# Kernel tuning notes

Measured on AMD Instinct MI355X. Metric: run time of the kernel, lower is better.

## Reference

```python
import jax, jax.numpy as jnp
import numpy as np

D_MODEL, N_HEAD, N_KV_HEAD, D_HEAD = 1024, 16, 4, 64


def rotate_half(x):
    x1, x2 = x[..., : x.shape[-1] // 2], x[..., x.shape[-1] // 2:]
    return jnp.concatenate((-x2, x1), axis=-1)


def rope_cos_sin(seq_len, dim, dtype=jnp.float32):
    inv_freq = 1.0 / (10000.0 ** (jnp.arange(0, dim, 2, dtype=jnp.float32) / dim))
    t = jnp.arange(seq_len, dtype=jnp.float32)
    freqs = jnp.einsum('i,j->ij', t, inv_freq)          # [S, dim/2]
    emb = jnp.concatenate((freqs, freqs), axis=-1)       # [S, dim]
    return jnp.cos(emb).astype(dtype), jnp.sin(emb).astype(dtype)


def setup_inputs() -> dict:
    key = jax.random.key(0)
    ks = jax.random.split(key, 5)
    B, S = 2, 2048
    scale = 0.02
    return {
        'x': jax.random.normal(ks[0], (B, S, D_MODEL), dtype=jnp.float32),
        'Wq': jax.random.normal(ks[1], (D_MODEL, N_HEAD * D_HEAD), dtype=jnp.float32) * scale,
        'Wk': jax.random.normal(ks[2], (D_MODEL, N_KV_HEAD * D_HEAD), dtype=jnp.float32) * scale,
        'Wv': jax.random.normal(ks[3], (D_MODEL, N_KV_HEAD * D_HEAD), dtype=jnp.float32) * scale,
        'Wo': jax.random.normal(ks[4], (N_HEAD * D_HEAD, D_MODEL), dtype=jnp.float32) * scale,
    }


def reference(x, Wq, Wk, Wv, Wo):
    B, S, _ = x.shape
    scale = 1.0 / np.sqrt(D_HEAD)
    # projections -> [B, H, S, Dh]
    q = (x @ Wq).reshape(B, S, N_HEAD, D_HEAD).transpose(0, 2, 1, 3)
    k = (x @ Wk).reshape(B, S, N_KV_HEAD, D_HEAD).transpose(0, 2, 1, 3)
    v = (x @ Wv).reshape(B, S, N_KV_HEAD, D_HEAD).transpose(0, 2, 1, 3)
    cos, sin = rope_cos_sin(S, D_HEAD, x.dtype)          # [S, Dh]
    q = q * cos + rotate_half(q) * sin
    k = k * cos + rotate_half(k) * sin
    rep = N_HEAD // N_KV_HEAD
    k = jnp.repeat(k, rep, axis=1)                       # [B, H, S, Dh]
    v = jnp.repeat(v, rep, axis=1)
    scores = jnp.einsum('bhqd,bhkd->bhqk', q, k) * scale # [B, H, S, S]
    causal = jnp.triu(jnp.ones((S, S), dtype=bool), k=1)
    scores = jnp.where(causal, -jnp.inf, scores)
    probs = jax.nn.softmax(scores, axis=-1)
    ctx = jnp.einsum('bhqk,bhkd->bhqd', probs, v)        # [B, H, S, Dh]
    ctx = ctx.transpose(0, 2, 1, 3).reshape(B, S, N_HEAD * D_HEAD)
    return ctx @ Wo
```

## Files before the change

kernel.cpp:

```cpp
#include <hip/hip_runtime.h>
#include <hip/hip_bf16.h>
#include <cstdint>
#include <math.h>

#define S_LEN 2048
#define DM 1024
#define NQKV 1536
#define MROWS 4096

typedef __attribute__((ext_vector_type(8))) short short8;
typedef __attribute__((ext_vector_type(4))) short short4v;
typedef __attribute__((ext_vector_type(4))) float f32x4;

#define MEMBAR() __asm__ __volatile__("" ::: "memory")

#define QFOLD 0.18033688011112042f

__device__ __forceinline__ short f2bf(float x) {
  union { float f; uint32_t u; } v; v.f = x;
  uint32_t r = (v.u + 0x7fffu + ((v.u >> 16) & 1u)) >> 16;
  return (short)(uint16_t)r;
}

__device__ __forceinline__ uint32_t pk2(float a, float b) {
  __hip_bfloat162 h = __float22bfloat162_rn(make_float2(a, b));
  union { __hip_bfloat162 h2; uint32_t u; } cv; cv.h2 = h;
  return cv.u;
}

__global__ void f32_to_bf16_vec(const float* __restrict__ in, short* __restrict__ out, int n4) {
  int i = blockIdx.x * blockDim.x + threadIdx.x;
  if (i < n4) {
    float4 v = ((const float4*)in)[i];
    short4 o;
    o.x = f2bf(v.x); o.y = f2bf(v.y); o.z = f2bf(v.z); o.w = f2bf(v.w);
    ((short4*)out)[i] = o;
  }
}

__global__ __launch_bounds__(256) void transpose_f32_bf16(const float* __restrict__ src,
    short* __restrict__ dst, int R, int C) {
  __shared__ short T[64 * 72];
  const int r0 = blockIdx.x * 64, c0 = blockIdx.y * 64;
  const int tid = threadIdx.x;
  #pragma unroll
  for (int i = 0; i < 4; ++i) {
    int chunk = tid + i * 256;
    int r = chunk >> 4, cc = (chunk & 15) * 4;
    float4 v = *(const float4*)&src[(size_t)(r0 + r) * C + c0 + cc];
    T[(cc + 0) * 72 + r] = f2bf(v.x);
    T[(cc + 1) * 72 + r] = f2bf(v.y);
    T[(cc + 2) * 72 + r] = f2bf(v.z);
    T[(cc + 3) * 72 + r] = f2bf(v.w);
  }
  __syncthreads();
  #pragma unroll
  for (int i = 0; i < 2; ++i) {
    int chunk = tid + i * 256;
    int rr = chunk >> 3, kk = (chunk & 7) * 8;
    *(uint4*)&dst[(size_t)(c0 + rr) * R + r0 + kk] = *(uint4*)&T[rr * 72 + kk];
  }
}

#define BM 128
#define BN 128
#define BKT 64

__global__ __launch_bounds__(256) void gemm_bf16(const short* __restrict__ A,
    const short* __restrict__ BT, float* __restrict__ C, int M, int N, int K) {
  __shared__ short As[BM * BKT];
  __shared__ short Bs[BN * BKT];
  const int tid = threadIdx.x;
  const int wave = tid >> 6, lane = tid & 63;
  const int quad = lane >> 4, l15 = lane & 15;
  const int wm = (wave >> 1) * 64, wn = (wave & 1) * 64;
  const int m0 = blockIdx.y * BM, n0 = blockIdx.x * BN;

  const int sr = wave * 32 + (lane >> 3);
  const int scol = (lane & 7) * 8;

  f32x4 acc[4][4] = {};

  for (int k0 = 0; k0 < K; k0 += BKT) {
    __syncthreads();
    #pragma unroll
    for (int j = 0; j < 4; ++j) {
      const int r = sr + j * 8;
      __builtin_amdgcn_global_load_lds(
          (const __attribute__((address_space(1))) void*)&A[(size_t)(m0 + r) * K + k0 + scol],
          (__attribute__((address_space(3))) void*)&As[(wave * 4 + j) * 512],
          16, 0, 0);
      __builtin_amdgcn_global_load_lds(
          (const __attribute__((address_space(1))) void*)&BT[(size_t)(n0 + r) * K + k0 + scol],
          (__attribute__((address_space(3))) void*)&Bs[(wave * 4 + j) * 512],
          16, 0, 0);
    }
    __syncthreads();
    #pragma unroll
    for (int ks = 0; ks < 2; ++ks) {
      short8 af[4], bfr[4];
      #pragma unroll
      for (int mi = 0; mi < 4; ++mi)
        af[mi] = *(const short8*)&As[(wm + mi*16 + l15)*BKT + ks*32 + quad*8];
      #pragma unroll
      for (int ni = 0; ni < 4; ++ni)
        bfr[ni] = *(const short8*)&Bs[(wn + ni*16 + l15)*BKT + ks*32 + quad*8];
      #pragma unroll
      for (int mi = 0; mi < 4; ++mi)
        #pragma unroll
        for (int ni = 0; ni < 4; ++ni)
          acc[mi][ni] = __builtin_amdgcn_mfma_f32_16x16x32_bf16(af[mi], bfr[ni], acc[mi][ni], 0, 0, 0);
    }
  }
  #pragma unroll
  for (int mi = 0; mi < 4; ++mi)
    #pragma unroll
    for (int ni = 0; ni < 4; ++ni)
      #pragma unroll
      for (int r = 0; r < 4; ++r)
        C[(size_t)(m0 + wm + mi*16 + quad*4 + r)*N + (n0 + wn + ni*16 + l15)] = acc[mi][ni][r];
}

__global__ void rope_kernel(const float* __restrict__ qkv, short* __restrict__ Qb,
                            short* __restrict__ Kb, short* __restrict__ Vb) {
  __shared__ float csn[64];
  const int row = blockIdx.x;
  const int s = row & (S_LEN - 1);
  const int tid = threadIdx.x;
  const float* rp = qkv + (size_t)row * NQKV;
  if (tid < 32) {
    float inv = exp2f(-(float)tid * 0.41524101186092029f);
    float ang = (float)s * inv;
    csn[tid] = cosf(ang);
    csn[tid + 32] = sinf(ang);
  }
  __syncthreads();
  #pragma unroll
  for (int i = 0; i < 2; ++i) {
    int p = tid + i * 256;
    int hh = p >> 5, j = p & 31;
    float cs = csn[j], sn = csn[j + 32];
    float x1 = rp[hh*64 + j], x2 = rp[hh*64 + j + 32];
    Qb[(size_t)row*1024 + hh*64 + j]      = f2bf((x1*cs - x2*sn) * QFOLD);
    Qb[(size_t)row*1024 + hh*64 + j + 32] = f2bf((x2*cs + x1*sn) * QFOLD);
  }
  if (tid < 128) {
    int hh = tid >> 5, j = tid & 31;
    float cs = csn[j], sn = csn[j + 32];
    float x1 = rp[1024 + hh*64 + j], x2 = rp[1024 + hh*64 + j + 32];
    Kb[(size_t)row*256 + hh*64 + j]      = f2bf(x1*cs - x2*sn);
    Kb[(size_t)row*256 + hh*64 + j + 32] = f2bf(x2*cs + x1*sn);
  }
  Vb[(size_t)row*256 + tid] = f2bf(rp[1280 + tid]);
}

__global__ __launch_bounds__(256) void transpose_v(const short* __restrict__ Vb,
                                                   short* __restrict__ Vt) {
  __shared__ short T[64 * 72];
  const int s0 = blockIdx.x * 64;
  const int bh = blockIdx.y;
  const int b = bh >> 2, kvh = bh & 3;
  const int tid = threadIdx.x;
  #pragma unroll
  for (int i = 0; i < 2; ++i) {
    int chunk = tid + i * 256;
    int r = chunk >> 3, c = (chunk & 7) * 8;
    short8 v = *(const short8*)&Vb[(size_t)(b*S_LEN + s0 + r)*256 + kvh*64 + c];
    #pragma unroll
    for (int t = 0; t < 8; ++t) T[(c + t) * 72 + r] = v[t];
  }
  __syncthreads();
  #pragma unroll
  for (int i = 0; i < 2; ++i) {
    int chunk = tid + i * 256;
    int rr = chunk >> 3, kk = (chunk & 7) * 8;
    *(uint4*)&Vt[(size_t)(bh*64 + rr)*S_LEN + s0 + kk] = *(uint4*)&T[rr * 72 + kk];
  }
}

#define PSTR 136

__global__ __launch_bounds__(256, 2) void fattn6(const short* __restrict__ Qb,
    const short* __restrict__ Kb, const short* __restrict__ Vt, short* __restrict__ Ctx) {
  __shared__ short Ks[128 * 72];
  __shared__ short Vts[64 * PSTR];
  __shared__ short Ps[4 * 16 * PSTR];
  const int idx = blockIdx.x;
  const int pi  = idx & 15;
  const int h   = (idx >> 4) & 15;
  const int b   = idx >> 8;
  const int kvh = h >> 2;
  const int tid = threadIdx.x, wave = tid >> 6, lane = tid & 63;
  const int quad = lane >> 4, l15 = lane & 15;
  const int roff = wave * 16;
  const size_t qbase  = (size_t)b * S_LEN * 1024;
  const size_t kbase  = (size_t)b * S_LEN * 256;
  const size_t vtbase = (size_t)(b*4 + kvh) * 64 * S_LEN;
  short* Psw = Ps + wave * 16 * PSTR;

  for (int half = 0; half < 2; ++half) {
    const int jt = half ? (31 - pi) : pi;
    const int q0 = jt * 64;
    const int ntiles = (jt >> 1) + 1;
    const int qrow = q0 + roff + l15;

    const short* qp = &Qb[qbase + (size_t)(q0 + roff + l15)*1024 + h*64 + quad*8];
    short8 qf0 = *(const short8*)qp;
    short8 qf1 = *(const short8*)(qp + 32);

    f32x4 O[4] = {};
    float ll = 0.f;

    short8 kreg[4], vreg[4];
    #pragma unroll
    for (int i = 0; i < 4; ++i) {
      int chunk = tid + i * 256;
      int kr = chunk >> 3, kc = (chunk & 7) * 8;
      kreg[i] = *(const short8*)&Kb[kbase + (size_t)kr*256 + kvh*64 + kc];
      int vr = chunk >> 4, vc = (chunk & 15) * 8;
      vreg[i] = *(const short8*)&Vt[vtbase + (size_t)vr*S_LEN + vc];
    }

    for (int t = 0; t < ntiles; ++t) {
      const int k0 = t * 128;
      __syncthreads();
      #pragma unroll
      for (int i = 0; i < 4; ++i) {
        int chunk = tid + i * 256;
        int kr = chunk >> 3, kc = (chunk & 7) * 8;
        *(short8*)&Ks[kr*72 + kc] = kreg[i];
        int vr = chunk >> 4, vc = (chunk & 15) * 8;
        *(short8*)&Vts[vr*PSTR + vc] = vreg[i];
      }
      __syncthreads();
      if (t + 1 < ntiles) {
        const int kn = (t + 1) * 128;
        #pragma unroll
        for (int i = 0; i < 4; ++i) {
          int chunk = tid + i * 256;
          int kr = chunk >> 3, kc = (chunk & 7) * 8;
          kreg[i] = *(const short8*)&Kb[kbase + (size_t)(kn + kr)*256 + kvh*64 + kc];
          int vr = chunk >> 4, vc = (chunk & 15) * 8;
          vreg[i] = *(const short8*)&Vt[vtbase + (size_t)vr*S_LEN + kn + vc];
        }
      }

      f32x4 sc[8];
      #pragma unroll
      for (int nt = 0; nt < 8; ++nt) {
        short8 kf0 = *(const short8*)&Ks[(nt*16 + l15)*72 + quad*8];
        short8 kf1 = *(const short8*)&Ks[(nt*16 + l15)*72 + 32 + quad*8];
        f32x4 a = {0.f, 0.f, 0.f, 0.f};
        a = __builtin_amdgcn_mfma_f32_16x16x32_bf16(kf0, qf0, a, 0, 0, 0);
        a = __builtin_amdgcn_mfma_f32_16x16x32_bf16(kf1, qf1, a, 0, 0, 0);
        sc[nt] = a;
      }
      if (t == ntiles - 1) {
        #pragma unroll
        for (int nt = 0; nt < 8; ++nt)
          #pragma unroll
          for (int r = 0; r < 4; ++r)
            if (k0 + nt*16 + quad*4 + r > qrow) sc[nt][r] = -1e30f;
      }
      #pragma unroll
      for (int nt = 0; nt < 8; ++nt) {
        float p0 = exp2f(sc[nt][0]);
        float p1 = exp2f(sc[nt][1]);
        float p2 = exp2f(sc[nt][2]);
        float p3 = exp2f(sc[nt][3]);
        ll += (p0 + p1) + (p2 + p3);
        union { uint2 uu; short4v s; } pkc;
        pkc.uu.x = pk2(p0, p1); pkc.uu.y = pk2(p2, p3);
        *(short4v*)&Psw[l15*PSTR + nt*16 + quad*4] = pkc.s;
      }
      MEMBAR();
      #pragma unroll
      for (int ks = 0; ks < 4; ++ks) {
        short8 a = *(const short8*)&Psw[l15*PSTR + ks*32 + quad*8];
        #pragma unroll
        for (int d = 0; d < 4; ++d) {
          short8 bv = *(const short8*)&Vts[(d*16 + l15)*PSTR + ks*32 + quad*8];
          O[d] = __builtin_amdgcn_mfma_f32_16x16x32_bf16(a, bv, O[d], 0, 0, 0);
        }
      }
    }

    ll += __shfl_xor(ll, 16, 64);
    ll += __shfl_xor(ll, 32, 64);
    #pragma unroll
    for (int r = 0; r < 4; ++r) {
      float lr = __shfl(ll, quad*4 + r, 64);
      float inv = 1.0f / lr;
      #pragma unroll
      for (int d = 0; d < 4; ++d) {
        int qr = q0 + roff + quad*4 + r;
        Ctx[qbase + (size_t)qr*1024 + h*64 + d*16 + l15] = f2bf(O[d][r] * inv);
      }
    }
  }
}

extern "C" void kernel_launch(void* const* d_in, const int* in_sizes, int n_in,
                              void* d_out, int out_size, void* d_ws, size_t ws_size,
                              hipStream_t stream) {
  const float* x  = (const float*)d_in[0];
  const float* Wq = (const float*)d_in[1];
  const float* Wk = (const float*)d_in[2];
  const float* Wv = (const float*)d_in[3];
  const float* Wo = (const float*)d_in[4];
  float* out = (float*)d_out;

  char* w = (char*)d_ws;
  short* Xb    = (short*)w;  w += (size_t)MROWS * DM * 2;
  short* WcatT = (short*)w;  w += (size_t)NQKV * DM * 2;
  short* WoT   = (short*)w;  w += (size_t)DM * DM * 2;
  float* QKVf  = (float*)w;  w += (size_t)MROWS * NQKV * 4;
  short* Qbuf  = (short*)w;  w += (size_t)MROWS * DM * 2;
  short* Kbuf  = (short*)w;  w += (size_t)MROWS * 256 * 2;
  short* Vbuf  = (short*)w;  w += (size_t)MROWS * 256 * 2;
  short* Vt    = (short*)w;  w += (size_t)8 * 64 * S_LEN * 2;
  short* Ctx   = (short*)QKVf;

  f32_to_bf16_vec<<<dim3(4096), dim3(256), 0, stream>>>(x, Xb, MROWS * DM / 4);
  transpose_f32_bf16<<<dim3(16, 16), dim3(256), 0, stream>>>(Wq, WcatT, 1024, 1024);
  transpose_f32_bf16<<<dim3(16, 4),  dim3(256), 0, stream>>>(Wk, WcatT + (size_t)1024*1024, 1024, 256);
  transpose_f32_bf16<<<dim3(16, 4),  dim3(256), 0, stream>>>(Wv, WcatT + (size_t)1280*1024, 1024, 256);
  transpose_f32_bf16<<<dim3(16, 16), dim3(256), 0, stream>>>(Wo, WoT, 1024, 1024);

  gemm_bf16<<<dim3(NQKV / BN, MROWS / BM), dim3(256), 0, stream>>>(Xb, WcatT, QKVf, MROWS, NQKV, DM);
  rope_kernel<<<dim3(MROWS), dim3(256), 0, stream>>>(QKVf, Qbuf, Kbuf, Vbuf);
  transpose_v<<<dim3(32, 8), dim3(256), 0, stream>>>(Vbuf, Vt);
  fattn6<<<dim3(512), dim3(256), 0, stream>>>(Qbuf, Kbuf, Vt, Ctx);
  gemm_bf16<<<dim3(DM / BN, MROWS / BM), dim3(256), 0, stream>>>(Ctx, WoT, out, MROWS, DM, DM);
}
```

Before: 195.5 us.

## Fuse RoPE and bf16 conversion into QKV GEMM epilogue; merge weight transposes

The QKV projection GEMM now applies RoPE, the Q scale fold and bf16 conversion in its epilogue and writes Q, K and V directly. This removes the fp32 QKV intermediate buffer and the separate rope kernel pass over it. The four weight-transpose launches are also merged into one launch. In exchange, each output element recomputes sin/cos per row in the GEMM epilogue, and the Ctx buffer now gets its own workspace region.

```diff
diff --git a/kernel.cpp b/kernel.cpp
--- a/kernel.cpp
+++ b/kernel.cpp
@@ -15,6 +15,7 @@
 #define MEMBAR() __asm__ __volatile__("" ::: "memory")
 
 #define QFOLD 0.18033688011112042f
+#define L2I 0.41524101186092029f
 
 __device__ __forceinline__ short f2bf(float x) {
   union { float f; uint32_t u; } v; v.f = x;
@@ -38,10 +39,17 @@
   }
 }
 
-__global__ __launch_bounds__(256) void transpose_f32_bf16(const float* __restrict__ src,
-    short* __restrict__ dst, int R, int C) {
+__global__ __launch_bounds__(256) void transpose_all(const float* __restrict__ Wq,
+    const float* __restrict__ Wk, const float* __restrict__ Wv, const float* __restrict__ Wo,
+    short* __restrict__ WcatT, short* __restrict__ WoT) {
   __shared__ short T[64 * 72];
-  const int r0 = blockIdx.x * 64, c0 = blockIdx.y * 64;
+  int t = blockIdx.x;
+  const float* src; short* dst; int C;
+  if (t < 256)      { src = Wq; dst = WcatT;                        C = 1024; }
+  else if (t < 320) { t -= 256; src = Wk; dst = WcatT + 1024*1024;  C = 256; }
+  else if (t < 384) { t -= 320; src = Wv; dst = WcatT + 1280*1024;  C = 256; }
+  else              { t -= 384; src = Wo; dst = WoT;                C = 1024; }
+  const int r0 = (t & 15) * 64, c0 = (t >> 4) * 64;
   const int tid = threadIdx.x;
   #pragma unroll
   for (int i = 0; i < 4; ++i) {
@@ -58,7 +66,7 @@
   for (int i = 0; i < 2; ++i) {
     int chunk = tid + i * 256;
     int rr = chunk >> 3, kk = (chunk & 7) * 8;
-    *(uint4*)&dst[(size_t)(c0 + rr) * R + r0 + kk] = *(uint4*)&T[rr * 72 + kk];
+    *(uint4*)&dst[(size_t)(c0 + rr) * 1024 + r0 + kk] = *(uint4*)&T[rr * 72 + kk];
   }
 }
 
@@ -66,8 +74,9 @@
 #define BN 128
 #define BKT 64
 
-__global__ __launch_bounds__(256) void gemm_bf16(const short* __restrict__ A,
-    const short* __restrict__ BT, float* __restrict__ C, int M, int N, int K) {
+__global__ __launch_bounds__(256) void gemm_qkv_rope(const short* __restrict__ A,
+    const short* __restrict__ BT, short* __restrict__ Qb, short* __restrict__ Kb,
+    short* __restrict__ Vb) {
   __shared__ short As[BM * BKT];
   __shared__ short Bs[BN * BKT];
   const int tid = threadIdx.x;
@@ -75,6 +84,7 @@
   const int quad = lane >> 4, l15 = lane & 15;
   const int wm = (wave >> 1) * 64, wn = (wave & 1) * 64;
   const int m0 = blockIdx.y * BM, n0 = blockIdx.x * BN;
+  const int K = DM;
 
   const int sr = wave * 32 + (lane >> 3);
   const int scol = (lane & 7) * 8;
@@ -112,6 +122,108 @@
           acc[mi][ni] = __builtin_amdgcn_mfma_f32_16x16x32_bf16(af[mi], bfr[ni], acc[mi][ni], 0, 0, 0);
     }
   }
+
+  const int colbase = n0 + wn;
+  const float inv0 = exp2f(-(float)l15 * L2I);
+  const float inv1 = exp2f(-(float)(l15 + 16) * L2I);
+
+  if (colbase < 1024) {
+    #pragma unroll
+    for (int mi = 0; mi < 4; ++mi)
+      #pragma unroll
+      for (int r = 0; r < 4; ++r) {
+        const int row = m0 + wm + mi*16 + quad*4 + r;
+        const int s = row & (S_LEN - 1);
+        float a0 = (float)s * inv0, a1 = (float)s * inv1;
+        float c0 = cosf(a0), s0 = sinf(a0);
+        float c1 = cosf(a1), s1 = sinf(a1);
+        size_t base = (size_t)row * 1024 + colbase + l15;
+        float x1 = acc[mi][0][r], x2 = acc[mi][2][r];
+        Qb[base +  0] = f2bf((x1*c0 - x2*s0) * QFOLD);
+        Qb[base + 32] = f2bf((x2*c0 + x1*s0) * QFOLD);
+        x1 = acc[mi][1][r]; x2 = acc[mi][3][r];
+        Qb[base + 16] = f2bf((x1*c1 - x2*s1) * QFOLD);
+        Qb[base + 48] = f2bf((x2*c1 + x1*s1) * QFOLD);
+      }
+  } else if (colbase < 1280) {
+    const int kcol = colbase - 1024;
+    #pragma unroll
+    for (int mi = 0; mi < 4; ++mi)
+      #pragma unroll
+      for (int r = 0; r < 4; ++r) {
+        const int row = m0 + wm + mi*16 + quad*4 + r;
+        const int s = row & (S_LEN - 1);
+        float a0 = (float)s * inv0, a1 = (float)s * inv1;
+        float c0 = cosf(a0), s0 = sinf(a0);
+        float c1 = cosf(a1), s1 = sinf(a1);
+        size_t base = (size_t)row * 256 + kcol + l15;
+        float x1 = acc[mi][0][r], x2 = acc[mi][2][r];
+        Kb[base +  0] = f2bf(x1*c0 - x2*s0);
+        Kb[base + 32] = f2bf(x2*c0 + x1*s0);
+        x1 = acc[mi][1][r]; x2 = acc[mi][3][r];
+        Kb[base + 16] = f2bf(x1*c1 - x2*s1);
+        Kb[base + 48] = f2bf(x2*c1 + x1*s1);
+      }
+  } else {
+    const int vcol = colbase - 1280;
+    #pragma unroll
+    for (int mi = 0; mi < 4; ++mi)
+      #pragma unroll
+      for (int ni = 0; ni < 4; ++ni)
+        #pragma unroll
+        for (int r = 0; r < 4; ++r) {
+          const int row = m0 + wm + mi*16 + quad*4 + r;
+          Vb[(size_t)row * 256 + vcol + ni*16 + l15] = f2bf(acc[mi][ni][r]);
+        }
+  }
+}
+
+__global__ __launch_bounds__(256) void gemm_bf16(const short* __restrict__ A,
+    const short* __restrict__ BT, float* __restrict__ C, int M, int N, int K) {
+  __shared__ short As[BM * BKT];
+  __shared__ short Bs[BN * BKT];
+  const int tid = threadIdx.x;
+  const int wave = tid >> 6, lane = tid & 63;
+  const int quad = lane >> 4, l15 = lane & 15;
+  const int wm = (wave >> 1) * 64, wn = (wave & 1) * 64;
+  const int m0 = blockIdx.y * BM, n0 = blockIdx.x * BN;
+
+  const int sr = wave * 32 + (lane >> 3);
+  const int scol = (lane & 7) * 8;
+
+  f32x4 acc[4][4] = {};
+
+  for (int k0 = 0; k0 < K; k0 += BKT) {
+    __syncthreads();
+    #pragma unroll
+    for (int j = 0; j < 4; ++j) {
+      const int r = sr + j * 8;
+      __builtin_amdgcn_global_load_lds(
+          (const __attribute__((address_space(1))) void*)&A[(size_t)(m0 + r) * K + k0 + scol],
+          (__attribute__((address_space(3))) void*)&As[(wave * 4 + j) * 512],
+          16, 0, 0);
+      __builtin_amdgcn_global_load_lds(
+          (const __attribute__((address_space(1))) void*)&BT[(size_t)(n0 + r) * K + k0 + scol],
+          (__attribute__((address_space(3))) void*)&Bs[(wave * 4 + j) * 512],
+          16, 0, 0);
+    }
+    __syncthreads();
+    #pragma unroll
+    for (int ks = 0; ks < 2; ++ks) {
+      short8 af[4], bfr[4];
+      #pragma unroll
+      for (int mi = 0; mi < 4; ++mi)
+        af[mi] = *(const short8*)&As[(wm + mi*16 + l15)*BKT + ks*32 + quad*8];
+      #pragma unroll
+      for (int ni = 0; ni < 4; ++ni)
+        bfr[ni] = *(const short8*)&Bs[(wn + ni*16 + l15)*BKT + ks*32 + quad*8];
+      #pragma unroll
+      for (int mi = 0; mi < 4; ++mi)
+        #pragma unroll
+        for (int ni = 0; ni < 4; ++ni)
+          acc[mi][ni] = __builtin_amdgcn_mfma_f32_16x16x32_bf16(af[mi], bfr[ni], acc[mi][ni], 0, 0, 0);
+    }
+  }
   #pragma unroll
   for (int mi = 0; mi < 4; ++mi)
     #pragma unroll
@@ -119,39 +231,6 @@
       #pragma unroll
       for (int r = 0; r < 4; ++r)
         C[(size_t)(m0 + wm + mi*16 + quad*4 + r)*N + (n0 + wn + ni*16 + l15)] = acc[mi][ni][r];
-}
-
-__global__ void rope_kernel(const float* __restrict__ qkv, short* __restrict__ Qb,
-                            short* __restrict__ Kb, short* __restrict__ Vb) {
-  __shared__ float csn[64];
-  const int row = blockIdx.x;
-  const int s = row & (S_LEN - 1);
-  const int tid = threadIdx.x;
-  const float* rp = qkv + (size_t)row * NQKV;
-  if (tid < 32) {
-    float inv = exp2f(-(float)tid * 0.41524101186092029f);
-    float ang = (float)s * inv;
-    csn[tid] = cosf(ang);
-    csn[tid + 32] = sinf(ang);
-  }
-  __syncthreads();
-  #pragma unroll
-  for (int i = 0; i < 2; ++i) {
-    int p = tid + i * 256;
-    int hh = p >> 5, j = p & 31;
-    float cs = csn[j], sn = csn[j + 32];
-    float x1 = rp[hh*64 + j], x2 = rp[hh*64 + j + 32];
-    Qb[(size_t)row*1024 + hh*64 + j]      = f2bf((x1*cs - x2*sn) * QFOLD);
-    Qb[(size_t)row*1024 + hh*64 + j + 32] = f2bf((x2*cs + x1*sn) * QFOLD);
-  }
-  if (tid < 128) {
-    int hh = tid >> 5, j = tid & 31;
-    float cs = csn[j], sn = csn[j + 32];
-    float x1 = rp[1024 + hh*64 + j], x2 = rp[1024 + hh*64 + j + 32];
-    Kb[(size_t)row*256 + hh*64 + j]      = f2bf(x1*cs - x2*sn);
-    Kb[(size_t)row*256 + hh*64 + j + 32] = f2bf(x2*cs + x1*sn);
-  }
-  Vb[(size_t)row*256 + tid] = f2bf(rp[1280 + tid]);
 }
 
 __global__ __launch_bounds__(256) void transpose_v(const short* __restrict__ Vb,
@@ -314,21 +393,15 @@
   short* Xb    = (short*)w;  w += (size_t)MROWS * DM * 2;
   short* WcatT = (short*)w;  w += (size_t)NQKV * DM * 2;
   short* WoT   = (short*)w;  w += (size_t)DM * DM * 2;
-  float* QKVf  = (float*)w;  w += (size_t)MROWS * NQKV * 4;
   short* Qbuf  = (short*)w;  w += (size_t)MROWS * DM * 2;
   short* Kbuf  = (short*)w;  w += (size_t)MROWS * 256 * 2;
   short* Vbuf  = (short*)w;  w += (size_t)MROWS * 256 * 2;
   short* Vt    = (short*)w;  w += (size_t)8 * 64 * S_LEN * 2;
-  short* Ctx   = (short*)QKVf;
+  short* Ctx   = (short*)w;  w += (size_t)MROWS * DM * 2;
 
   f32_to_bf16_vec<<<dim3(4096), dim3(256), 0, stream>>>(x, Xb, MROWS * DM / 4);
-  transpose_f32_bf16<<<dim3(16, 16), dim3(256), 0, stream>>>(Wq, WcatT, 1024, 1024);
-  transpose_f32_bf16<<<dim3(16, 4),  dim3(256), 0, stream>>>(Wk, WcatT + (size_t)1024*1024, 1024, 256);
-  transpose_f32_bf16<<<dim3(16, 4),  dim3(256), 0, stream>>>(Wv, WcatT + (size_t)1280*1024, 1024, 256);
-  transpose_f32_bf16<<<dim3(16, 16), dim3(256), 0, stream>>>(Wo, WoT, 1024, 1024);
-
-  gemm_bf16<<<dim3(NQKV / BN, MROWS / BM), dim3(256), 0, stream>>>(Xb, WcatT, QKVf, MROWS, NQKV, DM);
-  rope_kernel<<<dim3(MROWS), dim3(256), 0, stream>>>(QKVf, Qbuf, Kbuf, Vbuf);
+  transpose_all<<<dim3(640), dim3(256), 0, stream>>>(Wq, Wk, Wv, Wo, WcatT, WoT);
+  gemm_qkv_rope<<<dim3(NQKV / BN, MROWS / BM), dim3(256), 0, stream>>>(Xb, WcatT, Qbuf, Kbuf, Vbuf);
   transpose_v<<<dim3(32, 8), dim3(256), 0, stream>>>(Vbuf, Vt);
   fattn6<<<dim3(512), dim3(256), 0, stream>>>(Qbuf, Kbuf, Vt, Ctx);
   gemm_bf16<<<dim3(DM / BN, MROWS / BM), dim3(256), 0, stream>>>(Ctx, WoT, out, MROWS, DM, DM);
```

After: 351.4 us. 1.8x slower.
